# Optimization experiments

Hardware: AMD Instinct MI355X
Metric: run time of the kernel (lower is better)

## Reference

```python
import jax, jax.numpy as jnp
import numpy as np

K = 10
NUM_LAYERS = 2


def _lap_half_propagate(x, src, dst, w, n):
    """Compute (L_sym / 2) @ x where L = I - D^-1/2 A D^-1/2.
    w holds the scaled off-diagonal weights (-dinv[src]*dinv[dst]/2);
    self-loop diagonal of L/2 contributes 0.5*x."""
    agg = jax.ops.segment_sum(w[:, None] * x[src], dst, num_segments=n)
    return 0.5 * x + agg


def _bern_conv(x, src, dst, w, n, c):
    # Chebyshev-style recurrence as written in BernConv.forward
    tx0 = x
    tx1 = x - _lap_half_propagate(x, src, dst, w, n)
    out = c[0] * tx0 + c[1] * tx1
    for k in range(2, K + 1):
        tx2 = 2.0 * (tx1 - _lap_half_propagate(tx1, src, dst, w, n)) - tx0
        out = out + c[k] * tx2
        tx0, tx1 = tx1, tx2
    return out


def setup_inputs() -> dict:
    key = jax.random.key(0)
    ks = jax.random.split(key, 7)
    N, E, IN, H, OUT = 100000, 3200000, 256, 128, 64
    x = jax.random.normal(ks[0], (N, IN), dtype=jnp.float32)
    edge_index = jax.random.randint(ks[1], (2, E), 0, N, dtype=jnp.int64)
    W1 = jax.random.normal(ks[2], (IN, H), dtype=jnp.float32) / np.sqrt(IN)
    b1 = jax.random.normal(ks[3], (H,), dtype=jnp.float32) * 0.01
    coeffs = jax.random.uniform(ks[4], (NUM_LAYERS, K + 1), dtype=jnp.float32) / (K + 1)
    W2 = jax.random.normal(ks[5], (H, OUT), dtype=jnp.float32) / np.sqrt(H)
    b2 = jax.random.normal(ks[6], (OUT,), dtype=jnp.float32) * 0.01
    return {"x": x, "edge_index": edge_index, "W1": W1, "b1": b1,
            "coeffs": coeffs, "W2": W2, "b2": b2}


def reference(x, edge_index, W1, b1, coeffs, W2, b2):
    n = x.shape[0]
    src, dst = edge_index[0], edge_index[1]
    # symmetric normalized Laplacian off-diagonal weights (PyG get_laplacian, sym)
    deg = jax.ops.segment_sum(jnp.ones_like(src, dtype=x.dtype), src, num_segments=n)
    dinv = jnp.where(deg > 0, jax.lax.rsqrt(jnp.maximum(deg, 1e-30)), 0.0)
    w = -(dinv[src] * dinv[dst]) * 0.5  # edge_weight / 2 as in BernConv.forward

    h = jax.nn.relu(x @ W1 + b1)  # dropout omitted (eval mode)
    for l in range(NUM_LAYERS):
        h = jax.nn.relu(_bern_conv(h, src, dst, w, n, coeffs[l]))
    return h @ W2 + b2
```

## Files before the change

### kernel.cpp

```cpp
#include <hip/hip_runtime.h>
#include <hip/hip_fp16.h>


#define SCAN_BLOCK 256
#define SCAN_ITEMS 4
#define SCAN_CHUNK 1024

union h2cvt {
    float2 f2;
    __half2 h2[2];
};

__global__ __launch_bounds__(256) void hist_kernel(const int* __restrict__ src,
                                                   const int* __restrict__ dst,
                                                   int* __restrict__ deg_src,
                                                   int* __restrict__ cnt_dst, int E) {
    int stride = gridDim.x * blockDim.x;
    for (int e = blockIdx.x * blockDim.x + threadIdx.x; e < E; e += stride) {
        atomicAdd(&deg_src[src[e]], 1);
        atomicAdd(&cnt_dst[dst[e]], 1);
    }
}

__global__ __launch_bounds__(256) void dinv_kernel(const int* __restrict__ deg,
                                                   float* __restrict__ dinv, int n) {
    int i = blockIdx.x * blockDim.x + threadIdx.x;
    if (i < n) {
        int d = deg[i];
        dinv[i] = d > 0 ? rsqrtf((float)d) : 0.f;
    }
}

__global__ __launch_bounds__(SCAN_BLOCK) void scan_chunk_sum(const int* __restrict__ cnt,
                                                             int* __restrict__ bsum, int n) {
    __shared__ int sdata[SCAN_BLOCK];
    int tid = threadIdx.x;
    int base = blockIdx.x * SCAN_CHUNK + tid * SCAN_ITEMS;
    int s = 0;
    for (int i = 0; i < SCAN_ITEMS; ++i) {
        int idx = base + i;
        if (idx < n) s += cnt[idx];
    }
    sdata[tid] = s;
    __syncthreads();
    for (int off = SCAN_BLOCK / 2; off > 0; off >>= 1) {
        if (tid < off) sdata[tid] += sdata[tid + off];
        __syncthreads();
    }
    if (tid == 0) bsum[blockIdx.x] = sdata[0];
}

__global__ void scan_bsum(int* __restrict__ bsum, int nb) {
    if (threadIdx.x == 0 && blockIdx.x == 0) {
        int run = 0;
        for (int i = 0; i < nb; ++i) {
            int v = bsum[i];
            bsum[i] = run;
            run += v;
        }
    }
}

__global__ __launch_bounds__(SCAN_BLOCK) void scan_write(const int* __restrict__ cnt,
                                                         const int* __restrict__ bsum,
                                                         int* __restrict__ rowptr,
                                                         int* __restrict__ cursor,
                                                         int n, int total) {
    __shared__ int sdata[SCAN_BLOCK];
    int tid = threadIdx.x;
    int base = blockIdx.x * SCAN_CHUNK + tid * SCAN_ITEMS;
    int vals[SCAN_ITEMS];
    int s = 0;
    for (int i = 0; i < SCAN_ITEMS; ++i) {
        int idx = base + i;
        vals[i] = (idx < n) ? cnt[idx] : 0;
        s += vals[i];
    }
    sdata[tid] = s;
    __syncthreads();
    for (int off = 1; off < SCAN_BLOCK; off <<= 1) {
        int add = (tid >= off) ? sdata[tid - off] : 0;
        __syncthreads();
        sdata[tid] += add;
        __syncthreads();
    }
    int run = bsum[blockIdx.x] + sdata[tid] - s;
    for (int i = 0; i < SCAN_ITEMS; ++i) {
        int idx = base + i;
        if (idx < n) {
            rowptr[idx] = run;
            cursor[idx] = run;
        }
        run += vals[i];
    }
    if (blockIdx.x == 0 && tid == 0) rowptr[n] = total;
}

__global__ __launch_bounds__(256) void scatter_kernel(const int* __restrict__ src,
                                                      const int* __restrict__ dst,
                                                      const float* __restrict__ dinv,
                                                      int* __restrict__ cursor,
                                                      int2* __restrict__ colw, int E) {
    int stride = gridDim.x * blockDim.x;
    for (int e = blockIdx.x * blockDim.x + threadIdx.x; e < E; e += stride) {
        int s = src[e];
        int d = dst[e];
        float w = -0.5f * dinv[s] * dinv[d];
        int p = atomicAdd(&cursor[d], 1);
        int2 rec;
        rec.x = s;
        rec.y = __float_as_int(w);
        colw[p] = rec;
    }
}

__global__ __launch_bounds__(256) void tofp16_kernel(const float4* __restrict__ in,
                                                     float2* __restrict__ outh, int n4) {
    int stride = gridDim.x * blockDim.x;
    for (int i = blockIdx.x * blockDim.x + threadIdx.x; i < n4; i += stride) {
        float4 v = in[i];
        h2cvt c;
        c.h2[0] = __floats2half2_rn(v.x, v.y);
        c.h2[1] = __floats2half2_rn(v.z, v.w);
        outh[i] = c.f2;
    }
}

#define G1_ROWS 16
__global__ __launch_bounds__(128) void gemm1_kernel(const float* __restrict__ X,
                                                    const float* __restrict__ W,
                                                    const float* __restrict__ b,
                                                    float* __restrict__ H, int n) {
    __shared__ float xt[G1_ROWS][256];
    int j = threadIdx.x;
    int r0 = blockIdx.x * G1_ROWS;
    for (int i = threadIdx.x; i < G1_ROWS * 256; i += 128) {
        int r = i >> 8, k = i & 255;
        int row = r0 + r;
        xt[r][k] = (row < n) ? X[(size_t)row * 256 + k] : 0.f;
    }
    __syncthreads();
    float acc[G1_ROWS];
#pragma unroll
    for (int r = 0; r < G1_ROWS; ++r) acc[r] = 0.f;
    for (int k = 0; k < 256; ++k) {
        float wk = W[k * 128 + j];
#pragma unroll
        for (int r = 0; r < G1_ROWS; ++r) acc[r] += xt[r][k] * wk;
    }
    float bj = b[j];
    for (int r = 0; r < G1_ROWS; ++r) {
        int row = r0 + r;
        if (row < n) H[(size_t)row * 128 + j] = fmaxf(acc[r] + bj, 0.f);
    }
}

#define G2_ROWS 32
__global__ __launch_bounds__(64) void gemm2_kernel(const float* __restrict__ H,
                                                   const float* __restrict__ W,
                                                   const float* __restrict__ b,
                                                   float* __restrict__ O, int n) {
    __shared__ float xt[G2_ROWS][128];
    int j = threadIdx.x;
    int r0 = blockIdx.x * G2_ROWS;
    for (int i = threadIdx.x; i < G2_ROWS * 128; i += 64) {
        int r = i >> 7, k = i & 127;
        int row = r0 + r;
        xt[r][k] = (row < n) ? H[(size_t)row * 128 + k] : 0.f;
    }
    __syncthreads();
    float acc[G2_ROWS];
#pragma unroll
    for (int r = 0; r < G2_ROWS; ++r) acc[r] = 0.f;
    for (int k = 0; k < 128; ++k) {
        float wk = W[k * 64 + j];
#pragma unroll
        for (int r = 0; r < G2_ROWS; ++r) acc[r] += xt[r][k] * wk;
    }
    float bj = b[j];
    for (int r = 0; r < G2_ROWS; ++r) {
        int row = r0 + r;
        if (row < n) O[(size_t)row * 64 + j] = acc[r] + bj;
    }
}

__global__ __launch_bounds__(256) void prop_kernel(const float* __restrict__ XF,
                                                   const float2* __restrict__ XH,
                                                   float* __restrict__ T0,
                                                   float* __restrict__ OUT,
                                                   float* __restrict__ TX1,
                                                   float2* __restrict__ MH,
                                                   const int* __restrict__ rowptr,
                                                   const int2* __restrict__ colw,
                                                   const float* __restrict__ coeffs,
                                                   int cidx, int mode, int n) {
    int wave = (blockIdx.x * blockDim.x + threadIdx.x) >> 6;
    if (wave >= n) return;
    int lane = threadIdx.x & 63;
    int half = lane >> 5;
    int q = lane & 31;
    int v = wave;
    int start = rowptr[v];
    int end = rowptr[v + 1];

    float4 a0 = {0, 0, 0, 0}, a1 = {0, 0, 0, 0}, a2 = {0, 0, 0, 0}, a3 = {0, 0, 0, 0};

    for (int e0 = start; e0 < end; e0 += 64) {
        int m = end - e0;
        if (m > 64) m = 64;
        int sE = 0;
        float wE = 0.f;
        if (lane < m) {
            int2 rec = colw[e0 + lane];
            sE = rec.x;
            wE = __int_as_float(rec.y);
        }
        int iters = (m + 1) >> 1;
        int t = 0;
        for (; t + 4 <= iters; t += 4) {
            int j0 = 2 * t + half;
            int s0 = __shfl(sE, j0);
            int s1 = __shfl(sE, j0 + 2);
            int s2 = __shfl(sE, j0 + 4);
            int s3 = __shfl(sE, j0 + 6);
            float w0 = __shfl(wE, j0);
            float w1 = __shfl(wE, j0 + 2);
            float w2 = __shfl(wE, j0 + 4);
            float w3 = __shfl(wE, j0 + 6);
            h2cvt c0, c1, c2, c3;
            c0.f2 = XH[(size_t)s0 * 32 + q];
            c1.f2 = XH[(size_t)s1 * 32 + q];
            c2.f2 = XH[(size_t)s2 * 32 + q];
            c3.f2 = XH[(size_t)s3 * 32 + q];
            float2 lo, hi;
            lo = __half22float2(c0.h2[0]); hi = __half22float2(c0.h2[1]);
            a0.x += w0 * lo.x; a0.y += w0 * lo.y; a0.z += w0 * hi.x; a0.w += w0 * hi.y;
            lo = __half22float2(c1.h2[0]); hi = __half22float2(c1.h2[1]);
            a1.x += w1 * lo.x; a1.y += w1 * lo.y; a1.z += w1 * hi.x; a1.w += w1 * hi.y;
            lo = __half22float2(c2.h2[0]); hi = __half22float2(c2.h2[1]);
            a2.x += w2 * lo.x; a2.y += w2 * lo.y; a2.z += w2 * hi.x; a2.w += w2 * hi.y;
            lo = __half22float2(c3.h2[0]); hi = __half22float2(c3.h2[1]);
            a3.x += w3 * lo.x; a3.y += w3 * lo.y; a3.z += w3 * hi.x; a3.w += w3 * hi.y;
        }
        for (; t < iters; ++t) {
            int j0 = 2 * t + half;
            int s0 = __shfl(sE, j0);
            float w0 = __shfl(wE, j0);
            h2cvt c0;
            c0.f2 = XH[(size_t)s0 * 32 + q];
            float2 lo = __half22float2(c0.h2[0]);
            float2 hi = __half22float2(c0.h2[1]);
            a0.x += w0 * lo.x; a0.y += w0 * lo.y; a0.z += w0 * hi.x; a0.w += w0 * hi.y;
        }
    }
    float4 acc;
    acc.x = (a0.x + a1.x) + (a2.x + a3.x);
    acc.y = (a0.y + a1.y) + (a2.y + a3.y);
    acc.z = (a0.z + a1.z) + (a2.z + a3.z);
    acc.w = (a0.w + a1.w) + (a2.w + a3.w);
    acc.x += __shfl_xor(acc.x, 32);
    acc.y += __shfl_xor(acc.y, 32);
    acc.z += __shfl_xor(acc.z, 32);
    acc.w += __shfl_xor(acc.w, 32);

    if (half) return;

    size_t idx = (size_t)v * 32 + q;
    const float4* __restrict__ X4 = reinterpret_cast<const float4*>(XF);
    float4 self = X4[idx];
    float4 wr;

    if (mode == 0) {
        float c0 = coeffs[cidx];
        float c1 = coeffs[cidx + 1];
        wr.x = 0.5f * self.x - acc.x;
        wr.y = 0.5f * self.y - acc.y;
        wr.z = 0.5f * self.z - acc.z;
        wr.w = 0.5f * self.w - acc.w;
        reinterpret_cast<float4*>(TX1)[idx] = wr;
        float4 o;
        o.x = c0 * self.x + c1 * wr.x;
        o.y = c0 * self.y + c1 * wr.y;
        o.z = c0 * self.z + c1 * wr.z;
        o.w = c0 * self.w + c1 * wr.w;
        reinterpret_cast<float4*>(OUT)[idx] = o;
    } else {
        float ck = coeffs[cidx];
        float4 t0v = reinterpret_cast<const float4*>(T0)[idx];
        float4 t2;
        t2.x = self.x - 2.f * acc.x - t0v.x;
        t2.y = self.y - 2.f * acc.y - t0v.y;
        t2.z = self.z - 2.f * acc.z - t0v.z;
        t2.w = self.w - 2.f * acc.w - t0v.w;
        float4 o = reinterpret_cast<float4*>(OUT)[idx];
        o.x += ck * t2.x;
        o.y += ck * t2.y;
        o.z += ck * t2.z;
        o.w += ck * t2.w;
        if (mode == 1) {
            wr = t2;
            reinterpret_cast<float4*>(T0)[idx] = wr;
            reinterpret_cast<float4*>(OUT)[idx] = o;
        } else {
            wr.x = fmaxf(o.x, 0.f);
            wr.y = fmaxf(o.y, 0.f);
            wr.z = fmaxf(o.z, 0.f);
            wr.w = fmaxf(o.w, 0.f);
            reinterpret_cast<float4*>(T0)[idx] = wr;
        }
    }
    if (MH) {
        h2cvt c;
        c.h2[0] = __floats2half2_rn(wr.x, wr.y);
        c.h2[1] = __floats2half2_rn(wr.z, wr.w);
        MH[idx] = c.f2;
    }
}


extern "C" void kernel_launch(void* const* d_in, const int* in_sizes, int n_in,
                              void* d_out, int out_size, void* d_ws, size_t ws_size,
                              hipStream_t stream) {
    const float* x      = (const float*)d_in[0];
    const int*   ei     = (const int*)d_in[1];
    const float* W1     = (const float*)d_in[2];
    const float* b1     = (const float*)d_in[3];
    const float* coeffs = (const float*)d_in[4];
    const float* W2     = (const float*)d_in[5];
    const float* b2     = (const float*)d_in[6];
    float* out = (float*)d_out;

    const int n = in_sizes[0] / 256;
    const int E = in_sizes[1] / 2;
    const int* src = ei;
    const int* dst = ei + E;

    char* ws = (char*)d_ws;
    size_t off = 0;
    auto alloc = [&](size_t bytes) -> void* {
        off = (off + 255) & ~(size_t)255;
        void* p = (void*)(ws + off);
        off += bytes;
        return p;
    };
    size_t bufBytes = (size_t)n * 128 * sizeof(float);
    size_t mirBytes = (size_t)n * 128 * sizeof(__half);
    float*  bufA   = (float*)alloc(bufBytes);
    float*  bufB   = (float*)alloc(bufBytes);
    float*  bufC   = (float*)alloc(bufBytes);
    float2* mirA   = (float2*)alloc(mirBytes);
    float2* mirB   = (float2*)alloc(mirBytes);
    int2*   colw   = (int2*)alloc((size_t)E * sizeof(int2));
    int*    degs   = (int*)alloc((size_t)n * sizeof(int));
    int*    cntd   = (int*)alloc((size_t)n * sizeof(int));
    int*    rowptr = (int*)alloc((size_t)(n + 1) * sizeof(int));
    int*    cursor = (int*)alloc((size_t)n * sizeof(int));
    int*    bsum   = (int*)alloc(1024 * sizeof(int));
    float*  dinv   = (float*)alloc((size_t)n * sizeof(float));

    hipMemsetAsync(degs, 0, (size_t)n * sizeof(int), stream);
    hipMemsetAsync(cntd, 0, (size_t)n * sizeof(int), stream);

    hist_kernel<<<2048, 256, 0, stream>>>(src, dst, degs, cntd, E);
    dinv_kernel<<<(n + 255) / 256, 256, 0, stream>>>(degs, dinv, n);
    int nchunk = (n + SCAN_CHUNK - 1) / SCAN_CHUNK;
    scan_chunk_sum<<<nchunk, SCAN_BLOCK, 0, stream>>>(cntd, bsum, n);
    scan_bsum<<<1, 64, 0, stream>>>(bsum, nchunk);
    scan_write<<<nchunk, SCAN_BLOCK, 0, stream>>>(cntd, bsum, rowptr, cursor, n, E);
    scatter_kernel<<<4096, 256, 0, stream>>>(src, dst, dinv, cursor, colw, E);

    gemm1_kernel<<<(n + G1_ROWS - 1) / G1_ROWS, 128, 0, stream>>>(x, W1, b1, bufA, n);
    tofp16_kernel<<<2048, 256, 0, stream>>>((const float4*)bufA, mirA, n * 32);

    int pgrid = (n + 3) / 4;
    float*  A  = bufA;
    float*  B  = bufB;
    float*  C  = bufC;
    float2* mA = mirA;
    float2* mB = mirB;
    for (int l = 0; l < 2; ++l) {
        prop_kernel<<<pgrid, 256, 0, stream>>>(A, mA, A, C, B, mB, rowptr, colw,
                                               coeffs, l * 11 + 0, 0, n);
        float*  t0 = A;  float2* m0 = mA;
        float*  t1 = B;  float2* m1 = mB;
        for (int k = 2; k <= 9; ++k) {
            prop_kernel<<<pgrid, 256, 0, stream>>>(t1, m1, t0, C, nullptr, m0, rowptr,
                                                   colw, coeffs, l * 11 + k, 1, n);
            float* tf = t0; t0 = t1; t1 = tf;
            float2* tm = m0; m0 = m1; m1 = tm;
        }
        prop_kernel<<<pgrid, 256, 0, stream>>>(t1, m1, t0, C, nullptr,
                                               (l == 0) ? m0 : nullptr, rowptr,
                                               colw, coeffs, l * 11 + 10, 2, n);
        A = t0; mA = m0;
        B = t1; mB = m1;
    }

    gemm2_kernel<<<(n + G2_ROWS - 1) / G2_ROWS, 64, 0, stream>>>(A, W2, b2, out, n);
}
```

Before: 3.462 ms.

## Factor symmetric normalization into prescaled fp16 mirrors and drop per-edge weights

Per-edge weights are removed from the CSR: the fp16 feature mirror is prescaled by dinv[src], and the gather result is scaled by -0.5*dinv[dst] once per row. This halves the edge-record size (int instead of int2), removes the weight shuffles and multiplies in the inner loop, and lets the scatter kernel skip the dinv lookups. A zero pad row is added so inactive lanes index a valid row, and prescaling before fp16 rounding slightly changes numerics.

```diff
diff --git a/kernel.cpp b/kernel.cpp
--- a/kernel.cpp
+++ b/kernel.cpp
@@ -6,10 +6,9 @@
 #define SCAN_ITEMS 4
 #define SCAN_CHUNK 1024
 
-union h2cvt {
-    float2 f2;
-    __half2 h2[2];
-};
+typedef float fx2 __attribute__((ext_vector_type(2)));
+
+union f2h4 { fx2 f2; __half2 h2[2]; };
 
 __global__ __launch_bounds__(256) void hist_kernel(const int* __restrict__ src,
                                                    const int* __restrict__ dst,
@@ -98,32 +97,36 @@
 
 __global__ __launch_bounds__(256) void scatter_kernel(const int* __restrict__ src,
                                                       const int* __restrict__ dst,
-                                                      const float* __restrict__ dinv,
                                                       int* __restrict__ cursor,
-                                                      int2* __restrict__ colw, int E) {
+                                                      int* __restrict__ col, int E) {
     int stride = gridDim.x * blockDim.x;
     for (int e = blockIdx.x * blockDim.x + threadIdx.x; e < E; e += stride) {
-        int s = src[e];
         int d = dst[e];
-        float w = -0.5f * dinv[s] * dinv[d];
         int p = atomicAdd(&cursor[d], 1);
-        int2 rec;
-        rec.x = s;
-        rec.y = __float_as_int(w);
-        colw[p] = rec;
-    }
-}
-
-__global__ __launch_bounds__(256) void tofp16_kernel(const float4* __restrict__ in,
-                                                     float2* __restrict__ outh, int n4) {
+        col[p] = src[e];
+    }
+}
+
+__global__ __launch_bounds__(256) void mirror_kernel(const float4* __restrict__ src,
+                                                     fx2* __restrict__ dst,
+                                                     const float* __restrict__ dinv,
+                                                     int n4) {
     int stride = gridDim.x * blockDim.x;
     for (int i = blockIdx.x * blockDim.x + threadIdx.x; i < n4; i += stride) {
-        float4 v = in[i];
-        h2cvt c;
-        c.h2[0] = __floats2half2_rn(v.x, v.y);
-        c.h2[1] = __floats2half2_rn(v.z, v.w);
-        outh[i] = c.f2;
-    }
+        int v = i >> 5;
+        float dv = dinv[v];
+        float4 x = src[i];
+        f2h4 u;
+        u.h2[0] = __floats2half2_rn(x.x * dv, x.y * dv);
+        u.h2[1] = __floats2half2_rn(x.z * dv, x.w * dv);
+        dst[i] = u.f2;
+    }
+}
+
+__global__ void pad_kernel(float* __restrict__ mA, float* __restrict__ mB, int n) {
+    int t = threadIdx.x;
+    if (t < 64) mA[(size_t)n * 64 + t] = 0.f;
+    else mB[(size_t)n * 64 + (t - 64)] = 0.f;
 }
 
 #define G1_ROWS 16
@@ -185,13 +188,14 @@
 }
 
 __global__ __launch_bounds__(256) void prop_kernel(const float* __restrict__ XF,
-                                                   const float2* __restrict__ XH,
+                                                   const fx2* __restrict__ XH,
                                                    float* __restrict__ T0,
                                                    float* __restrict__ OUT,
                                                    float* __restrict__ TX1,
-                                                   float2* __restrict__ MH,
+                                                   fx2* __restrict__ MH,
                                                    const int* __restrict__ rowptr,
-                                                   const int2* __restrict__ colw,
+                                                   const int* __restrict__ col,
+                                                   const float* __restrict__ dinv,
                                                    const float* __restrict__ coeffs,
                                                    int cidx, int mode, int n) {
     int wave = (blockIdx.x * blockDim.x + threadIdx.x) >> 6;
@@ -208,13 +212,8 @@
     for (int e0 = start; e0 < end; e0 += 64) {
         int m = end - e0;
         if (m > 64) m = 64;
-        int sE = 0;
-        float wE = 0.f;
-        if (lane < m) {
-            int2 rec = colw[e0 + lane];
-            sE = rec.x;
-            wE = __int_as_float(rec.y);
-        }
+        int sE = n;
+        if (lane < m) sE = col[e0 + lane];
         int iters = (m + 1) >> 1;
         int t = 0;
         for (; t + 4 <= iters; t += 4) {
@@ -223,34 +222,29 @@
             int s1 = __shfl(sE, j0 + 2);
             int s2 = __shfl(sE, j0 + 4);
             int s3 = __shfl(sE, j0 + 6);
-            float w0 = __shfl(wE, j0);
-            float w1 = __shfl(wE, j0 + 2);
-            float w2 = __shfl(wE, j0 + 4);
-            float w3 = __shfl(wE, j0 + 6);
-            h2cvt c0, c1, c2, c3;
+            f2h4 c0, c1, c2, c3;
             c0.f2 = XH[(size_t)s0 * 32 + q];
             c1.f2 = XH[(size_t)s1 * 32 + q];
             c2.f2 = XH[(size_t)s2 * 32 + q];
             c3.f2 = XH[(size_t)s3 * 32 + q];
             float2 lo, hi;
             lo = __half22float2(c0.h2[0]); hi = __half22float2(c0.h2[1]);
-            a0.x += w0 * lo.x; a0.y += w0 * lo.y; a0.z += w0 * hi.x; a0.w += w0 * hi.y;
+            a0.x += lo.x; a0.y += lo.y; a0.z += hi.x; a0.w += hi.y;
             lo = __half22float2(c1.h2[0]); hi = __half22float2(c1.h2[1]);
-            a1.x += w1 * lo.x; a1.y += w1 * lo.y; a1.z += w1 * hi.x; a1.w += w1 * hi.y;
+            a1.x += lo.x; a1.y += lo.y; a1.z += hi.x; a1.w += hi.y;
             lo = __half22float2(c2.h2[0]); hi = __half22float2(c2.h2[1]);
-            a2.x += w2 * lo.x; a2.y += w2 * lo.y; a2.z += w2 * hi.x; a2.w += w2 * hi.y;
+            a2.x += lo.x; a2.y += lo.y; a2.z += hi.x; a2.w += hi.y;
             lo = __half22float2(c3.h2[0]); hi = __half22float2(c3.h2[1]);
-            a3.x += w3 * lo.x; a3.y += w3 * lo.y; a3.z += w3 * hi.x; a3.w += w3 * hi.y;
+            a3.x += lo.x; a3.y += lo.y; a3.z += hi.x; a3.w += hi.y;
         }
         for (; t < iters; ++t) {
             int j0 = 2 * t + half;
             int s0 = __shfl(sE, j0);
-            float w0 = __shfl(wE, j0);
-            h2cvt c0;
+            f2h4 c0;
             c0.f2 = XH[(size_t)s0 * 32 + q];
             float2 lo = __half22float2(c0.h2[0]);
             float2 hi = __half22float2(c0.h2[1]);
-            a0.x += w0 * lo.x; a0.y += w0 * lo.y; a0.z += w0 * hi.x; a0.w += w0 * hi.y;
+            a0.x += lo.x; a0.y += lo.y; a0.z += hi.x; a0.w += hi.y;
         }
     }
     float4 acc;
@@ -265,6 +259,13 @@
 
     if (half) return;
 
+    float dv = dinv[v];
+    float sw = -0.5f * dv;
+    float gx = sw * acc.x;
+    float gy = sw * acc.y;
+    float gz = sw * acc.z;
+    float gw = sw * acc.w;
+
     size_t idx = (size_t)v * 32 + q;
     const float4* __restrict__ X4 = reinterpret_cast<const float4*>(XF);
     float4 self = X4[idx];
@@ -273,10 +274,10 @@
     if (mode == 0) {
         float c0 = coeffs[cidx];
         float c1 = coeffs[cidx + 1];
-        wr.x = 0.5f * self.x - acc.x;
-        wr.y = 0.5f * self.y - acc.y;
-        wr.z = 0.5f * self.z - acc.z;
-        wr.w = 0.5f * self.w - acc.w;
+        wr.x = 0.5f * self.x - gx;
+        wr.y = 0.5f * self.y - gy;
+        wr.z = 0.5f * self.z - gz;
+        wr.w = 0.5f * self.w - gw;
         reinterpret_cast<float4*>(TX1)[idx] = wr;
         float4 o;
         o.x = c0 * self.x + c1 * wr.x;
@@ -288,10 +289,10 @@
         float ck = coeffs[cidx];
         float4 t0v = reinterpret_cast<const float4*>(T0)[idx];
         float4 t2;
-        t2.x = self.x - 2.f * acc.x - t0v.x;
-        t2.y = self.y - 2.f * acc.y - t0v.y;
-        t2.z = self.z - 2.f * acc.z - t0v.z;
-        t2.w = self.w - 2.f * acc.w - t0v.w;
+        t2.x = self.x - 2.f * gx - t0v.x;
+        t2.y = self.y - 2.f * gy - t0v.y;
+        t2.z = self.z - 2.f * gz - t0v.z;
+        t2.w = self.w - 2.f * gw - t0v.w;
         float4 o = reinterpret_cast<float4*>(OUT)[idx];
         o.x += ck * t2.x;
         o.y += ck * t2.y;
@@ -310,10 +311,10 @@
         }
     }
     if (MH) {
-        h2cvt c;
-        c.h2[0] = __floats2half2_rn(wr.x, wr.y);
-        c.h2[1] = __floats2half2_rn(wr.z, wr.w);
-        MH[idx] = c.f2;
+        f2h4 u;
+        u.h2[0] = __floats2half2_rn(wr.x * dv, wr.y * dv);
+        u.h2[1] = __floats2half2_rn(wr.z * dv, wr.w * dv);
+        MH[idx] = u.f2;
     }
 }
 
@@ -344,22 +345,22 @@
         return p;
     };
     size_t bufBytes = (size_t)n * 128 * sizeof(float);
-    size_t mirBytes = (size_t)n * 128 * sizeof(__half);
-    float*  bufA   = (float*)alloc(bufBytes);
-    float*  bufB   = (float*)alloc(bufBytes);
-    float*  bufC   = (float*)alloc(bufBytes);
-    float2* mirA   = (float2*)alloc(mirBytes);
-    float2* mirB   = (float2*)alloc(mirBytes);
-    int2*   colw   = (int2*)alloc((size_t)E * sizeof(int2));
-    int*    degs   = (int*)alloc((size_t)n * sizeof(int));
-    int*    cntd   = (int*)alloc((size_t)n * sizeof(int));
-    int*    rowptr = (int*)alloc((size_t)(n + 1) * sizeof(int));
-    int*    cursor = (int*)alloc((size_t)n * sizeof(int));
-    int*    bsum   = (int*)alloc(1024 * sizeof(int));
-    float*  dinv   = (float*)alloc((size_t)n * sizeof(float));
-
-    hipMemsetAsync(degs, 0, (size_t)n * sizeof(int), stream);
-    hipMemsetAsync(cntd, 0, (size_t)n * sizeof(int), stream);
+    size_t mirBytes = (size_t)(n + 1) * 128 * sizeof(__half);
+    float* bufA   = (float*)alloc(bufBytes);
+    float* bufB   = (float*)alloc(bufBytes);
+    float* bufC   = (float*)alloc(bufBytes);
+    fx2*   mirA   = (fx2*)alloc(mirBytes);
+    fx2*   mirB   = (fx2*)alloc(mirBytes);
+    int*   col    = (int*)alloc((size_t)E * sizeof(int));
+    int*   degs   = (int*)alloc((size_t)n * sizeof(int));
+    int*   cntd   = (int*)alloc((size_t)n * sizeof(int));
+    int*   rowptr = (int*)alloc((size_t)(n + 1) * sizeof(int));
+    int*   cursor = (int*)alloc((size_t)n * sizeof(int));
+    int*   bsum   = (int*)alloc(1024 * sizeof(int));
+    float* dinv   = (float*)alloc((size_t)n * sizeof(float));
+
+    (void)hipMemsetAsync(degs, 0, (size_t)n * sizeof(int), stream);
+    (void)hipMemsetAsync(cntd, 0, (size_t)n * sizeof(int), stream);
 
     hist_kernel<<<2048, 256, 0, stream>>>(src, dst, degs, cntd, E);
     dinv_kernel<<<(n + 255) / 256, 256, 0, stream>>>(degs, dinv, n);
@@ -367,31 +368,32 @@
     scan_chunk_sum<<<nchunk, SCAN_BLOCK, 0, stream>>>(cntd, bsum, n);
     scan_bsum<<<1, 64, 0, stream>>>(bsum, nchunk);
     scan_write<<<nchunk, SCAN_BLOCK, 0, stream>>>(cntd, bsum, rowptr, cursor, n, E);
-    scatter_kernel<<<4096, 256, 0, stream>>>(src, dst, dinv, cursor, colw, E);
+    scatter_kernel<<<4096, 256, 0, stream>>>(src, dst, cursor, col, E);
 
     gemm1_kernel<<<(n + G1_ROWS - 1) / G1_ROWS, 128, 0, stream>>>(x, W1, b1, bufA, n);
-    tofp16_kernel<<<2048, 256, 0, stream>>>((const float4*)bufA, mirA, n * 32);
+    mirror_kernel<<<2048, 256, 0, stream>>>((const float4*)bufA, mirA, dinv, n * 32);
+    pad_kernel<<<1, 128, 0, stream>>>((float*)mirA, (float*)mirB, n);
 
     int pgrid = (n + 3) / 4;
-    float*  A  = bufA;
-    float*  B  = bufB;
-    float*  C  = bufC;
-    float2* mA = mirA;
-    float2* mB = mirB;
+    float* A  = bufA;
+    float* B  = bufB;
+    float* C  = bufC;
+    fx2*   mA = mirA;
+    fx2*   mB = mirB;
     for (int l = 0; l < 2; ++l) {
-        prop_kernel<<<pgrid, 256, 0, stream>>>(A, mA, A, C, B, mB, rowptr, colw,
+        prop_kernel<<<pgrid, 256, 0, stream>>>(A, mA, A, C, B, mB, rowptr, col, dinv,
                                                coeffs, l * 11 + 0, 0, n);
-        float*  t0 = A;  float2* m0 = mA;
-        float*  t1 = B;  float2* m1 = mB;
+        float* t0 = A;  fx2* m0 = mA;
+        float* t1 = B;  fx2* m1 = mB;
         for (int k = 2; k <= 9; ++k) {
             prop_kernel<<<pgrid, 256, 0, stream>>>(t1, m1, t0, C, nullptr, m0, rowptr,
-                                                   colw, coeffs, l * 11 + k, 1, n);
+                                                   col, dinv, coeffs, l * 11 + k, 1, n);
             float* tf = t0; t0 = t1; t1 = tf;
-            float2* tm = m0; m0 = m1; m1 = tm;
+            fx2* tm = m0; m0 = m1; m1 = tm;
         }
         prop_kernel<<<pgrid, 256, 0, stream>>>(t1, m1, t0, C, nullptr,
-                                               (l == 0) ? m0 : nullptr, rowptr,
-                                               colw, coeffs, l * 11 + 10, 2, n);
+                                               (l == 0) ? m0 : nullptr, rowptr, col,
+                                               dinv, coeffs, l * 11 + 10, 2, n);
         A = t0; mA = m0;
         B = t1; mB = m1;
     }
```

Measured after the change: 3.530 ms. About the same (+2.0%).
